# Performance work log

Hardware: AMD Instinct MI355X
Metric: run time of the kernel (lower is better)

The kernel has to match this reference:

```python
import jax, jax.numpy as jnp
import numpy as np
from jax import lax

B, T, TP = 16, 128, 32
V, E, H = 256, 128, 256


def _lstm_step(x, h, c, Wih, Whh, bih, bhh):
    # PyTorch nn.LSTM gate math, gate order i, f, g, o
    g = x @ Wih.T + bih + h @ Whh.T + bhh  # (BT, 4H)
    i, f, gg, o = jnp.split(g, 4, axis=-1)
    i = jax.nn.sigmoid(i)
    f = jax.nn.sigmoid(f)
    gg = jnp.tanh(gg)
    o = jax.nn.sigmoid(o)
    c = f * c + i * gg
    h = o * jnp.tanh(c)
    return h, c


def setup_inputs() -> dict:
    key = jax.random.key(0)
    ks = jax.random.split(key, 14)
    s = 0.05
    return {
        "phonemes": jax.random.randint(ks[0], (B, T, TP), 0, V, dtype=jnp.int32),
        "phoneme_lengths": jax.random.randint(ks[1], (B, T), 1, TP + 1, dtype=jnp.int32),
        "emb": jax.random.normal(ks[2], (V, E), jnp.float32) * s,
        "enc_Wih": jax.random.normal(ks[3], (4 * H, E), jnp.float32) * s,
        "enc_Whh": jax.random.normal(ks[4], (4 * H, H), jnp.float32) * s,
        "enc_bih": jax.random.normal(ks[5], (4 * H,), jnp.float32) * s,
        "enc_bhh": jax.random.normal(ks[6], (4 * H,), jnp.float32) * s,
        "dec_Wih": jax.random.normal(ks[7], (4 * H, E), jnp.float32) * s,
        "dec_Whh": jax.random.normal(ks[8], (4 * H, H), jnp.float32) * s,
        "dec_bih": jax.random.normal(ks[9], (4 * H,), jnp.float32) * s,
        "dec_bhh": jax.random.normal(ks[10], (4 * H,), jnp.float32) * s,
        "fc_W": jax.random.normal(ks[11], (V, H), jnp.float32) * s,
        "fc_b": jax.random.normal(ks[12], (V,), jnp.float32) * s,
        "sos_token": 1,
    }


def reference(phonemes, phoneme_lengths, emb, enc_Wih, enc_Whh, enc_bih, enc_bhh,
              dec_Wih, dec_Whh, dec_bih, dec_bhh, fc_W, fc_b, sos_token):
    b, t, tp = phonemes.shape
    bt = b * t
    hid = enc_Whh.shape[1]
    dt = emb.dtype

    # ---- encoder: embedding + LSTM over T_phoneme, gather last valid state ----
    x = emb[phonemes.reshape(bt, tp)]            # (BT, TP, E)
    h0 = jnp.zeros((bt, hid), dt)
    c0 = jnp.zeros((bt, hid), dt)

    def enc_step(carry, xt):
        h, c = carry
        h, c = _lstm_step(xt, h, c, enc_Wih, enc_Whh, enc_bih, enc_bhh)
        return (h, c), h

    _, hs = lax.scan(enc_step, (h0, c0), jnp.transpose(x, (1, 0, 2)))  # (TP, BT, H)
    lens = phoneme_lengths.reshape(bt)
    last_idx = jnp.clip(lens.astype(jnp.int32) - 1, 0, tp - 1)
    enc_last = hs[last_idx, jnp.arange(bt)]      # (BT, H) = decoder initial h

    tok0 = jnp.full((bt,), sos_token, jnp.int32)

    def dec_step(carry, _):
        h, c, tok = carry
        xt = emb[tok]                            # (BT, E)
        h, c = _lstm_step(xt, h, c, dec_Wih, dec_Whh, dec_bih, dec_bhh)
        scores = h @ fc_W.T + fc_b               # (BT, V)
        tok = jnp.argmax(scores, axis=-1).astype(jnp.int32)
        return (h, c, tok), scores

    _, scores = lax.scan(dec_step, (enc_last, jnp.zeros_like(enc_last), tok0),
                         None, length=tp)        # (TP, BT, V)
    return jnp.transpose(scores, (1, 0, 2))      # (BT, TP, V), matching torch output
```

## Files before the change

kernel.cpp:

```cpp
#include <hip/hip_runtime.h>
#include <math.h>

#define Hn   256
#define En   128
#define Vn   256
#define TPn  32
#define BTn  2048
#define NSV  8
#define NWG  (BTn / NSV)
#define NT   1024
#define SROW2 258

#define KATTR __attribute__((amdgpu_flat_work_group_size(1024, 1024), amdgpu_waves_per_eu(4, 4)))

typedef __attribute__((ext_vector_type(8))) short bf16x8;
typedef __attribute__((ext_vector_type(4))) float f32x4;
typedef __attribute__((ext_vector_type(2))) float f32x2;

__device__ __forceinline__ float sigf(float x) {
    return __builtin_amdgcn_rcpf(1.0f + __expf(-x));
}
__device__ __forceinline__ float tanh_fast(float x) {
    float e = __expf(2.0f * x);
    return 1.0f - 2.0f * __builtin_amdgcn_rcpf(e + 1.0f);
}
__device__ __forceinline__ unsigned bf16rne(float x) {
    unsigned b = __float_as_uint(x);
    return (b + 0x7FFFu + ((b >> 16) & 1u)) >> 16;
}
__device__ __forceinline__ unsigned pk2(float a, float b) {
    return bf16rne(a) | (bf16rne(b) << 16);
}
__device__ __forceinline__ float bfu(unsigned short x) {
    return __uint_as_float(((unsigned)x) << 16);
}
__device__ __forceinline__ unsigned long long amax_key(float sc, int v) {
    unsigned fb = __float_as_uint(sc);
    fb = (fb & 0x80000000u) ? ~fb : (fb | 0x80000000u);
    return ((unsigned long long)fb << 32) | (unsigned)(Vn - 1 - v);
}
__device__ __forceinline__ float dot4(float4 a, float4 b, float acc) {
    return fmaf(a.x, b.x, fmaf(a.y, b.y, fmaf(a.z, b.z, fmaf(a.w, b.w, acc))));
}


__global__ void make_ptab(float4* __restrict__ Pp, const float* __restrict__ emb,
                          const float* __restrict__ Wih, const float* __restrict__ bih,
                          const float* __restrict__ bhh) {
    int v = blockIdx.x, u = threadIdx.x;
    __shared__ __align__(16) float es[En];
    if (u < En) es[u] = emb[v * En + u];
    __syncthreads();
    float a[4];
#pragma unroll
    for (int g = 0; g < 4; ++g) {
        int r = g * Hn + u;
        float acc = bih[r] + bhh[r];
        const float4* w4 = (const float4*)(Wih + r * En);
        const float4* e4 = (const float4*)es;
        for (int k = 0; k < En / 4; ++k) acc = dot4(w4[k], e4[k], acc);
        a[g] = acc;
    }
    Pp[v * Hn + u] = make_float4(a[0], a[1], a[2], a[3]);
}

__global__ void pack_afrag(uint4* __restrict__ A, const float* __restrict__ Whh,
                           const float* __restrict__ fcW, int ntile) {
    int idx = blockIdx.x * 256 + threadIdx.x;
    if (idx >= ntile * 512) return;
    int l = idx & 63, q = (idx >> 6) & 7, t = idx >> 9;
    int r = 16 * t + (l & 15);
    int kb = 32 * q + 8 * (l >> 4);
    const float* s = (r < 1024) ? (Whh + r * Hn + kb) : (fcW + (r - 1024) * Hn + kb);
    A[idx] = make_uint4(pk2(s[0], s[1]), pk2(s[2], s[3]), pk2(s[4], s[5]), pk2(s[6], s[7]));
}

__global__ KATTR void enc_kernel(
    const bf16x8* __restrict__ AW, const float4* __restrict__ Ptu,
    const int* __restrict__ phon, const int* __restrict__ lens,
    float* __restrict__ h0dec) {
    const int tid = threadIdx.x, wg = blockIdx.x;
    const int wv = tid >> 6, l = tid & 63;
    const int c16 = l & 15, rg = l >> 4;
    const int u = tid >> 2, ch = tid & 3;
    const int sA = 2 * ch, sB = 2 * ch + 1;
    __shared__ __align__(16) bf16x8 resW[128 * 64];
    __shared__ __align__(16) uint4 hBf[8 * 64];
    __shared__ unsigned short gactG[1024 * 8];
    __shared__ int lsh[NSV];

    if (tid < 512) hBf[tid] = make_uint4(0u, 0u, 0u, 0u);
    if (tid < NSV) lsh[tid] = lens[wg * NSV + tid];
#pragma unroll
    for (int q = 0; q < 8; ++q)
        resW[(wv * 8 + q) * 64 + l] = AW[((4 * wv) * 8 + q) * 64 + l];
    float cA = 0.f, cB = 0.f;
    __syncthreads();
    int mx = 0;
#pragma unroll
    for (int i = 0; i < NSV; ++i) mx = max(mx, lsh[i]);
    const int lenA = lsh[sA], lenB = lsh[sB];

    const bf16x8* AWw = AW + (4 * wv) * 512 + l;

    for (int t = 0; t < mx; ++t) {
        const int tokA = phon[(wg * NSV + sA) * TPn + t];
        const int tokB = phon[(wg * NSV + sB) * TPn + t];

        f32x4 acc[4];
#pragma unroll
        for (int ii = 0; ii < 4; ++ii) acc[ii] = (f32x4){0.f, 0.f, 0.f, 0.f};
#pragma unroll
        for (int q = 0; q < 8; ++q) {
            bf16x8 bf = *(const bf16x8*)&hBf[q * 64 + l];
            acc[0] = __builtin_amdgcn_mfma_f32_16x16x32_bf16(
                resW[(wv * 8 + q) * 64 + l], bf, acc[0], 0, 0, 0);
#pragma unroll
            for (int ii = 1; ii < 4; ++ii) {
                acc[ii] = __builtin_amdgcn_mfma_f32_16x16x32_bf16(
                    AWw[ii * 512 + q * 64], bf, acc[ii], 0, 0, 0);
            }
        }
        const float4 pA = Ptu[tokA * Hn + u];
        const float4 pB = Ptu[tokB * Hn + u];
        if (c16 < 8) {
#pragma unroll
            for (int ii = 0; ii < 4; ++ii) {
                int Rb = (4 * wv + ii) * 16 + rg * 4;
#pragma unroll
                for (int r = 0; r < 4; ++r)
                    gactG[(Rb + r) * 8 + c16] = (unsigned short)bf16rne(acc[ii][r]);
            }
        }
        __syncthreads();

        float g0A = bfu(gactG[(u) * 8 + sA]),         g0B = bfu(gactG[(u) * 8 + sB]);
        float g1A = bfu(gactG[(256 + u) * 8 + sA]),   g1B = bfu(gactG[(256 + u) * 8 + sB]);
        float g2A = bfu(gactG[(512 + u) * 8 + sA]),   g2B = bfu(gactG[(512 + u) * 8 + sB]);
        float g3A = bfu(gactG[(768 + u) * 8 + sA]),   g3B = bfu(gactG[(768 + u) * 8 + sB]);
        float hvA, hvB;
        {
            float gi = sigf(g0A + pA.x), gf = sigf(g1A + pA.y);
            float gg = tanh_fast(g2A + pA.z), go = sigf(g3A + pA.w);
            cA = fmaf(gf, cA, gi * gg); hvA = go * tanh_fast(cA);
        }
        {
            float gi = sigf(g0B + pB.x), gf = sigf(g1B + pB.y);
            float gg = tanh_fast(g2B + pB.z), go = sigf(g3B + pB.w);
            cB = fmaf(gf, cB, gi * gg); hvB = go * tanh_fast(cB);
        }
        if (t == lenA - 1) __builtin_nontemporal_store(hvA, &h0dec[(wg * NSV + sA) * Hn + u]);
        if (t == lenB - 1) __builtin_nontemporal_store(hvB, &h0dec[(wg * NSV + sB) * Hn + u]);
        {
            unsigned short* hb16 = (unsigned short*)hBf;
            int q = u >> 5, g = (u >> 3) & 3, j = u & 7;
            hb16[(q * 64 + g * 16 + sA) * 8 + j] = (unsigned short)bf16rne(hvA);
            hb16[(q * 64 + g * 16 + sB) * 8 + j] = (unsigned short)bf16rne(hvB);
        }
        __syncthreads();
    }
}

__global__ KATTR void dec_kernel(
    const bf16x8* __restrict__ AW, const float4* __restrict__ Ptu,
    const float* __restrict__ fcb, const float* __restrict__ h0dec,
    const int* __restrict__ sosp, float* __restrict__ out) {
    const int tid = threadIdx.x, wg = blockIdx.x;
    const int wv = tid >> 6, l = tid & 63;
    const int c16 = l & 15, rg = l >> 4;
    const int u = tid >> 2, ch = tid & 3;
    const int sA = 2 * ch, sB = 2 * ch + 1;
    __shared__ __align__(16) bf16x8 resW[127 * 64];
    __shared__ __align__(16) uint4 hBf[8 * 64];
    __shared__ unsigned short gactG[1024 * 8];
    __shared__ float scx[NSV * SROW2];
    __shared__ unsigned long long gmax[2][NSV];

    if (tid < 512) {
        int q = tid >> 6, ll = tid & 63, c = ll & 15, g = ll >> 4;
        uint4 v = make_uint4(0u, 0u, 0u, 0u);
        if (c < 8) {
            const float* hp = h0dec + (wg * NSV + c) * Hn + 32 * q + 8 * g;
            float4 v0 = *(const float4*)hp;
            float4 v1 = *(const float4*)(hp + 4);
            v = make_uint4(pk2(v0.x, v0.y), pk2(v0.z, v0.w), pk2(v1.x, v1.y), pk2(v1.z, v1.w));
        }
        hBf[tid] = v;
    }
    if (tid < 2 * NSV) ((unsigned long long*)gmax)[tid] = 0ull;
#pragma unroll
    for (int q = 0; q < 8; ++q)
        if (wv < 15 || q < 7)
            resW[(wv * 8 + q) * 64 + l] = AW[((5 * wv) * 8 + q) * 64 + l];
    const int sos0 = sosp[0];
    float cA = 0.f, cB = 0.f;
    __syncthreads();

    const bf16x8* AWw = AW + (5 * wv) * 512 + l;

    for (int i = 0; i <= TPn; ++i) {
        const bool full = (i < TPn);

        f32x4 acc[5];
#pragma unroll
        for (int ii = 0; ii < 5; ++ii) {
            const int t5 = 5 * wv + ii;
            if (t5 >= 64) {
                acc[ii] = *(const f32x4*)&fcb[(t5 - 64) * 16 + rg * 4];
            } else {
                acc[ii] = (f32x4){0.f, 0.f, 0.f, 0.f};
            }
        }
#pragma unroll
        for (int q = 0; q < 8; ++q) {
            bf16x8 bf = *(const bf16x8*)&hBf[q * 64 + l];
            bf16x8 a0 = (wv < 15 || q < 7) ? resW[(wv * 8 + q) * 64 + l] : AWw[q * 64];
            acc[0] = __builtin_amdgcn_mfma_f32_16x16x32_bf16(a0, bf, acc[0], 0, 0, 0);
#pragma unroll
            for (int ii = 1; ii < 5; ++ii) {
                acc[ii] = __builtin_amdgcn_mfma_f32_16x16x32_bf16(
                    AWw[ii * 512 + q * 64], bf, acc[ii], 0, 0, 0);
            }
        }
        if (c16 < 8) {
#pragma unroll
            for (int ii = 0; ii < 5; ++ii) {
                const int t5 = 5 * wv + ii;
                if (t5 < 64) {
                    int Rb = t5 * 16 + rg * 4;
#pragma unroll
                    for (int r = 0; r < 4; ++r)
                        gactG[(Rb + r) * 8 + c16] = (unsigned short)bf16rne(acc[ii][r]);
                }
            }
        }
        if (i > 0) {
            unsigned long long kbest = 0ull;
            if (c16 < 8) {
#pragma unroll
                for (int ii = 0; ii < 5; ++ii) {
                    const int t5 = 5 * wv + ii;
                    if (t5 >= 64) {
                        int vb = (t5 - 64) * 16 + rg * 4;
#pragma unroll
                        for (int r = 0; r < 4; ++r) {
                            float sc = acc[ii][r];
                            scx[c16 * SROW2 + vb + r] = sc;
                            unsigned long long k = amax_key(sc, vb + r);
                            if (k > kbest) kbest = k;
                        }
                    }
                }
            }
            if (wv >= 12) {
                unsigned long long o = __shfl_xor(kbest, 16, 64); if (o > kbest) kbest = o;
                o = __shfl_xor(kbest, 32, 64); if (o > kbest) kbest = o;
                if (c16 < 8 && rg == 0) atomicMax(&gmax[i & 1][c16], kbest);
            }
        }
        __syncthreads();

        int tokA = sos0, tokB = sos0;
        if (i > 0) {
            {
                int s = tid >> 7, k = (tid & 127) * 2;
                f32x2 v = *(const f32x2*)&scx[s * SROW2 + k];
                __builtin_nontemporal_store(
                    v, (f32x2*)&out[((long)(wg * NSV + s) * TPn + (i - 1)) * Vn + k]);
            }
            tokA = (Vn - 1) - (int)(gmax[i & 1][sA] & 0xffffffffu);
            tokB = (Vn - 1) - (int)(gmax[i & 1][sB] & 0xffffffffu);
            if (tid < NSV) gmax[(i + 1) & 1][tid] = 0ull;
        }

        if (full) {
            const float4 pA = Ptu[tokA * Hn + u];
            const float4 pB = Ptu[tokB * Hn + u];
            float g0A = bfu(gactG[(u) * 8 + sA]),       g0B = bfu(gactG[(u) * 8 + sB]);
            float g1A = bfu(gactG[(256 + u) * 8 + sA]), g1B = bfu(gactG[(256 + u) * 8 + sB]);
            float g2A = bfu(gactG[(512 + u) * 8 + sA]), g2B = bfu(gactG[(512 + u) * 8 + sB]);
            float g3A = bfu(gactG[(768 + u) * 8 + sA]), g3B = bfu(gactG[(768 + u) * 8 + sB]);
            float hvA, hvB;
            {
                float gi = sigf(g0A + pA.x), gf = sigf(g1A + pA.y);
                float gg = tanh_fast(g2A + pA.z), go = sigf(g3A + pA.w);
                cA = fmaf(gf, cA, gi * gg); hvA = go * tanh_fast(cA);
            }
            {
                float gi = sigf(g0B + pB.x), gf = sigf(g1B + pB.y);
                float gg = tanh_fast(g2B + pB.z), go = sigf(g3B + pB.w);
                cB = fmaf(gf, cB, gi * gg); hvB = go * tanh_fast(cB);
            }
            unsigned short* hb16 = (unsigned short*)hBf;
            int q = u >> 5, g = (u >> 3) & 3, j = u & 7;
            hb16[(q * 64 + g * 16 + sA) * 8 + j] = (unsigned short)bf16rne(hvA);
            hb16[(q * 64 + g * 16 + sB) * 8 + j] = (unsigned short)bf16rne(hvB);
        }
        __syncthreads();
    }
}

extern "C" void kernel_launch(void* const* d_in, const int* in_sizes, int n_in,
                              void* d_out, int out_size, void* d_ws, size_t ws_size,
                              hipStream_t stream) {
    const int*   phon = (const int*)d_in[0];
    const int*   lens = (const int*)d_in[1];
    const float* emb  = (const float*)d_in[2];
    const float* eWih = (const float*)d_in[3];
    const float* eWhh = (const float*)d_in[4];
    const float* ebih = (const float*)d_in[5];
    const float* ebhh = (const float*)d_in[6];
    const float* dWih = (const float*)d_in[7];
    const float* dWhh = (const float*)d_in[8];
    const float* dbih = (const float*)d_in[9];
    const float* dbhh = (const float*)d_in[10];
    const float* fcW  = (const float*)d_in[11];
    const float* fcb  = (const float*)d_in[12];
    const int*   sos  = (const int*)d_in[13];
    float* out = (float*)d_out;

    float4* Ptu_e = (float4*)d_ws;
    float4* Ptu_d = Ptu_e + 65536;
    uint4*  AW_e  = (uint4*)(Ptu_d + 65536);
    uint4*  AW_d  = AW_e + 32768;
    float*  h0d   = (float*)(AW_d + 40960);

    make_ptab<<<256, 256, 0, stream>>>(Ptu_e, emb, eWih, ebih, ebhh);
    make_ptab<<<256, 256, 0, stream>>>(Ptu_d, emb, dWih, dbih, dbhh);
    pack_afrag<<<128, 256, 0, stream>>>(AW_e, eWhh, eWhh, 64);
    pack_afrag<<<160, 256, 0, stream>>>(AW_d, dWhh, fcW, 80);
    enc_kernel<<<NWG, NT, 0, stream>>>((const bf16x8*)AW_e, Ptu_e, phon, lens, h0d);
    dec_kernel<<<NWG, NT, 0, stream>>>((const bf16x8*)AW_d, Ptu_d, fcb, h0d, sos, out);
}
```

Measured before the change: 876.1 us.

## Spread argmax over all threads via LDS staging of fc scores

The fc score tiles are now written to a padded float LDS buffer instead of being reduced in place by the last four waves. After a new barrier, every thread reads two scores, adds the bias, writes them out and runs a wave-wide shuffle reduction before the atomicMax. Gate preloads move before the second barrier, and the resident weight cache shrinks to 7 q-slices per wave, so the last slice always streams from global memory. This balances the argmax work across all waves but adds an extra __syncthreads per step and more LDS traffic.

```diff
diff --git a/kernel.cpp b/kernel.cpp
--- a/kernel.cpp
+++ b/kernel.cpp
@@ -10,6 +10,7 @@
 #define NWG  (BTn / NSV)
 #define NT   1024
 #define SROW2 258
+#define RESQ_D 7
 
 #define KATTR __attribute__((amdgpu_flat_work_group_size(1024, 1024), amdgpu_waves_per_eu(4, 4)))
 
@@ -170,9 +171,11 @@
     const int c16 = l & 15, rg = l >> 4;
     const int u = tid >> 2, ch = tid & 3;
     const int sA = 2 * ch, sB = 2 * ch + 1;
-    __shared__ __align__(16) bf16x8 resW[127 * 64];
+    const int ln = tid & 63;
+    __shared__ __align__(16) bf16x8 resW[16 * RESQ_D * 64];
     __shared__ __align__(16) uint4 hBf[8 * 64];
     __shared__ unsigned short gactG[1024 * 8];
+    __shared__ float gactF[256 * 9];
     __shared__ float scx[NSV * SROW2];
     __shared__ unsigned long long gmax[2][NSV];
 
@@ -189,10 +192,10 @@
     }
     if (tid < 2 * NSV) ((unsigned long long*)gmax)[tid] = 0ull;
 #pragma unroll
-    for (int q = 0; q < 8; ++q)
-        if (wv < 15 || q < 7)
-            resW[(wv * 8 + q) * 64 + l] = AW[((5 * wv) * 8 + q) * 64 + l];
+    for (int q = 0; q < RESQ_D; ++q)
+        resW[(wv * RESQ_D + q) * 64 + l] = AW[((5 * wv) * 8 + q) * 64 + l];
     const int sos0 = sosp[0];
+    const float fb = fcb[u];
     float cA = 0.f, cB = 0.f;
     __syncthreads();
 
@@ -203,18 +206,11 @@
 
         f32x4 acc[5];
 #pragma unroll
-        for (int ii = 0; ii < 5; ++ii) {
-            const int t5 = 5 * wv + ii;
-            if (t5 >= 64) {
-                acc[ii] = *(const f32x4*)&fcb[(t5 - 64) * 16 + rg * 4];
-            } else {
-                acc[ii] = (f32x4){0.f, 0.f, 0.f, 0.f};
-            }
-        }
+        for (int ii = 0; ii < 5; ++ii) acc[ii] = (f32x4){0.f, 0.f, 0.f, 0.f};
 #pragma unroll
         for (int q = 0; q < 8; ++q) {
             bf16x8 bf = *(const bf16x8*)&hBf[q * 64 + l];
-            bf16x8 a0 = (wv < 15 || q < 7) ? resW[(wv * 8 + q) * 64 + l] : AWw[q * 64];
+            bf16x8 a0 = (q < RESQ_D) ? resW[(wv * RESQ_D + q) * 64 + l] : AWw[q * 64];
             acc[0] = __builtin_amdgcn_mfma_f32_16x16x32_bf16(a0, bf, acc[0], 0, 0, 0);
 #pragma unroll
             for (int ii = 1; ii < 5; ++ii) {
@@ -226,36 +222,45 @@
 #pragma unroll
             for (int ii = 0; ii < 5; ++ii) {
                 const int t5 = 5 * wv + ii;
+                const int Rb = t5 * 16 + rg * 4;
                 if (t5 < 64) {
-                    int Rb = t5 * 16 + rg * 4;
 #pragma unroll
                     for (int r = 0; r < 4; ++r)
                         gactG[(Rb + r) * 8 + c16] = (unsigned short)bf16rne(acc[ii][r]);
+                } else {
+#pragma unroll
+                    for (int r = 0; r < 4; ++r)
+                        gactF[(Rb - 1024 + r) * 9 + c16] = acc[ii][r];
                 }
             }
         }
+        __syncthreads();
+
+        float g0A = 0.f, g1A = 0.f, g2A = 0.f, g3A = 0.f;
+        float g0B = 0.f, g1B = 0.f, g2B = 0.f, g3B = 0.f;
+        if (full) {
+            g0A = bfu(gactG[(u) * 8 + sA]);       g0B = bfu(gactG[(u) * 8 + sB]);
+            g1A = bfu(gactG[(256 + u) * 8 + sA]); g1B = bfu(gactG[(256 + u) * 8 + sB]);
+            g2A = bfu(gactG[(512 + u) * 8 + sA]); g2B = bfu(gactG[(512 + u) * 8 + sB]);
+            g3A = bfu(gactG[(768 + u) * 8 + sA]); g3B = bfu(gactG[(768 + u) * 8 + sB]);
+        }
         if (i > 0) {
-            unsigned long long kbest = 0ull;
-            if (c16 < 8) {
-#pragma unroll
-                for (int ii = 0; ii < 5; ++ii) {
-                    const int t5 = 5 * wv + ii;
-                    if (t5 >= 64) {
-                        int vb = (t5 - 64) * 16 + rg * 4;
-#pragma unroll
-                        for (int r = 0; r < 4; ++r) {
-                            float sc = acc[ii][r];
-                            scx[c16 * SROW2 + vb + r] = sc;
-                            unsigned long long k = amax_key(sc, vb + r);
-                            if (k > kbest) kbest = k;
-                        }
-                    }
-                }
-            }
-            if (wv >= 12) {
-                unsigned long long o = __shfl_xor(kbest, 16, 64); if (o > kbest) kbest = o;
-                o = __shfl_xor(kbest, 32, 64); if (o > kbest) kbest = o;
-                if (c16 < 8 && rg == 0) atomicMax(&gmax[i & 1][c16], kbest);
+            float scA = gactF[u * 9 + sA] + fb;
+            float scB = gactF[u * 9 + sB] + fb;
+            scx[sA * SROW2 + u] = scA;
+            scx[sB * SROW2 + u] = scB;
+            unsigned long long kA = amax_key(scA, u);
+            unsigned long long kB = amax_key(scB, u);
+#pragma unroll
+            for (int off = 4; off < 64; off <<= 1) {
+                unsigned long long oA = __shfl_xor(kA, off, 64);
+                unsigned long long oB = __shfl_xor(kB, off, 64);
+                if (oA > kA) kA = oA;
+                if (oB > kB) kB = oB;
+            }
+            if (ln < 4) {
+                atomicMax(&gmax[i & 1][sA], kA);
+                atomicMax(&gmax[i & 1][sB], kB);
             }
         }
         __syncthreads();
@@ -276,10 +281,6 @@
         if (full) {
             const float4 pA = Ptu[tokA * Hn + u];
             const float4 pB = Ptu[tokB * Hn + u];
-            float g0A = bfu(gactG[(u) * 8 + sA]),       g0B = bfu(gactG[(u) * 8 + sB]);
-            float g1A = bfu(gactG[(256 + u) * 8 + sA]), g1B = bfu(gactG[(256 + u) * 8 + sB]);
-            float g2A = bfu(gactG[(512 + u) * 8 + sA]), g2B = bfu(gactG[(512 + u) * 8 + sB]);
-            float g3A = bfu(gactG[(768 + u) * 8 + sA]), g3B = bfu(gactG[(768 + u) * 8 + sB]);
             float hvA, hvB;
             {
                 float gi = sigf(g0A + pA.x), gf = sigf(g1A + pA.y);
```

Result: no change. 863.2 us (-1.5%).
